# Kernel optimization log

Measured on AMD Instinct MI355X. Metric: run time of the kernel, lower is better.

Reference implementation:

```python
import jax, jax.numpy as jnp
import numpy as np
from jax import lax

B, T, S = 64, 4096, 64


def setup_inputs() -> dict:
    key = jax.random.key(0)
    k1, k2, k3 = jax.random.split(key, 3)
    transition_potentials = jax.random.normal(k1, (S, S), dtype=jnp.float32)
    emission_potentials = jax.random.normal(k2, (B, T, S), dtype=jnp.float32)
    seq_lens = jax.random.randint(k3, (B,), 1, T + 1)
    return {
        "transition_potentials": transition_potentials,
        "emission_potentials": emission_potentials,
        "seq_lens": seq_lens,
    }


def reference(transition_potentials, emission_potentials, seq_lens):
    # potential_normalization='none', potential_scale=1.0 -> normalize is identity.
    # HMM forward algorithm: alpha[t] = logsumexp_i(alpha[t-1,i] + A[i,j]) + emis[t]
    alpha0 = emission_potentials[:, 0, :]  # [B,S]

    def step(alpha_prev, emis_t):
        # alpha_prev: [B,S]; emis_t: [B,S]; transition: [S,S]
        alpha_t = jax.nn.logsumexp(
            alpha_prev[:, :, None] + transition_potentials[None, :, :], axis=1
        ) + emis_t
        return alpha_t, alpha_t

    emis_rest = jnp.moveaxis(emission_potentials[:, 1:, :], 1, 0)  # [T-1,B,S]
    _, alphas = lax.scan(step, alpha0, emis_rest)  # [T-1,B,S]
    alpha = jnp.concatenate([alpha0[None], alphas], axis=0)  # [T,B,S]
    alpha = jnp.moveaxis(alpha, 0, 1)  # [B,T,S]
    log_Z = jax.nn.logsumexp(alpha[:, -1, :], axis=-1)  # [B]
    return alpha, log_Z
```

## Files before the change

kernel.cpp:

```cpp
#include <hip/hip_runtime.h>
#include <hip/hip_bf16.h>


#define BB 64
#define TT 4096
#define SS 64
#define C_CH 128
#define LL 32
#define WARM 24
#define PF 8

typedef __attribute__((ext_vector_type(4))) short bh4;
typedef __attribute__((ext_vector_type(4))) float f32x4;

#define LOG2E 1.44269504088896340736f
#define LN2F  0.69314718055994530942f

__device__ __forceinline__ float fexp2(float x) {
#if __has_builtin(__builtin_amdgcn_exp2f)
    return __builtin_amdgcn_exp2f(x);
#else
    return exp2f(x);
#endif
}
__device__ __forceinline__ float flog2(float x) {
#if __has_builtin(__builtin_amdgcn_logf)
    return __builtin_amdgcn_logf(x);
#else
    return log2f(x);
#endif
}
__device__ __forceinline__ float bpermf(int idx, float v) {
    return __uint_as_float((unsigned)__builtin_amdgcn_ds_bpermute(idx, (int)__float_as_uint(v)));
}
__device__ __forceinline__ int pack_bf16(float x, float y) {
    __hip_bfloat162 h = __float22bfloat162_rn(make_float2(x, y));
    int r; __builtin_memcpy(&r, &h, 4); return r;
}
union PB2 { int i[2]; bh4 v; };

__device__ __forceinline__ f32x4 mfma16(bh4 a, bh4 b, f32x4 c) {
#if __has_builtin(__builtin_amdgcn_mfma_f32_16x16x16bf16_1k)
    return __builtin_amdgcn_mfma_f32_16x16x16bf16_1k(a, b, c, 0, 0, 0);
#else
    asm("v_mfma_f32_16x16x16_bf16 %0, %1, %2, %0" : "+v"(c) : "v"(a), "v"(b));
    return c;
#endif
}

__device__ __forceinline__ float do_step(f32x4 (&al2)[4], const f32x4 (&er)[4],
                                         const bh4 (&Af)[4][4],
                                         float M2, int idxM) {
    bh4 Bf[4];
    #pragma unroll
    for (int kb = 0; kb < 4; ++kb) {
        PB2 pb;
        pb.i[0] = pack_bf16(fexp2(al2[kb].x - M2), fexp2(al2[kb].y - M2));
        pb.i[1] = pack_bf16(fexp2(al2[kb].z - M2), fexp2(al2[kb].w - M2));
        Bf[kb] = pb.v;
    }

    float M2n = 0.f;
    #pragma unroll
    for (int jt = 0; jt < 4; ++jt) {
        f32x4 d0 = {0.f, 0.f, 0.f, 0.f};
        f32x4 d1 = {0.f, 0.f, 0.f, 0.f};
        d0 = mfma16(Af[jt][0], Bf[0], d0);
        d1 = mfma16(Af[jt][1], Bf[1], d1);
        d0 = mfma16(Af[jt][2], Bf[2], d0);
        d1 = mfma16(Af[jt][3], Bf[3], d1);
        f32x4 d = d0 + d1;
        al2[jt].x = fmaf(er[jt].x, LOG2E, M2) + flog2(d.x);
        al2[jt].y = fmaf(er[jt].y, LOG2E, M2) + flog2(d.y);
        al2[jt].z = fmaf(er[jt].z, LOG2E, M2) + flog2(d.z);
        al2[jt].w = fmaf(er[jt].w, LOG2E, M2) + flog2(d.w);
        if (jt == 0) M2n = bpermf(idxM, al2[0].x);
    }
    return M2n;
}

__device__ __forceinline__ void load_row(f32x4 (&dst)[4],
                                         const float* __restrict__ eb,
                                         int t, int off) {
    const float* p = eb + (t & (TT - 1)) * SS + off;
    #pragma unroll
    for (int jt = 0; jt < 4; ++jt)
        dst[jt] = *(const f32x4*)(p + 16 * jt);
}

__global__ __launch_bounds__(64)
__attribute__((amdgpu_waves_per_eu(1, 1)))
void hmm_phaseA(const float* __restrict__ trans,
                const float* __restrict__ emis,
                float* __restrict__ out,
                float* __restrict__ ws_warm,
                float* __restrict__ ws_bound) {
    const int lane = threadIdx.x;
    const int n = lane & 15, q = lane >> 4;
    const int w = blockIdx.x;
    const int b = w >> 3, cg = w & 7;
    const int c = 16 * cg + n;
    const bool is_c0 = (c == 0);
    const int off = 4 * q;

    bh4 Af[4][4];
    #pragma unroll
    for (int jt = 0; jt < 4; ++jt)
        #pragma unroll
        for (int kb = 0; kb < 4; ++kb) {
            float v0 = __expf(trans[(16 * kb + 4 * q + 0) * SS + 16 * jt + n]);
            float v1 = __expf(trans[(16 * kb + 4 * q + 1) * SS + 16 * jt + n]);
            float v2 = __expf(trans[(16 * kb + 4 * q + 2) * SS + 16 * jt + n]);
            float v3 = __expf(trans[(16 * kb + 4 * q + 3) * SS + 16 * jt + n]);
            PB2 pb;
            pb.i[0] = pack_bf16(v0, v1);
            pb.i[1] = pack_bf16(v2, v3);
            Af[jt][kb] = pb.v;
        }

    const int idxM = n << 2;

    const float* eb = emis + (size_t)b * TT * SS;
    float*       ob = out  + (size_t)b * TT * SS;

    const int t0 = LL * c - (WARM + 1);

    f32x4 al2[4], e0[4], ebuf[PF][4];
    load_row(al2, eb, t0, off);
    #pragma unroll
    for (int jt = 0; jt < 4; ++jt) al2[jt] = al2[jt] * LOG2E;
    load_row(e0, eb, 0, off);
    #pragma unroll
    for (int k = 0; k < PF; ++k) load_row(ebuf[k], eb, t0 + 1 + k, off);

    float M2 = bpermf(idxM, al2[0].x);

    #pragma unroll 1
    for (int g = 0; g < 3; ++g) {
        #pragma unroll
        for (int k = 0; k < PF; ++k) {
            int s = PF * g + k + 1;
            f32x4 er[4];
            #pragma unroll
            for (int jt = 0; jt < 4; ++jt) er[jt] = ebuf[k][jt];
            load_row(ebuf[k], eb, t0 + s + PF, off);
            M2 = do_step(al2, er, Af, M2, idxM);
        }
    }
    if (lane < 16)
        ws_warm[b * C_CH + 16 * cg + lane] = al2[0].x * LN2F;

    #pragma unroll 1
    for (int g = 0; g < 4; ++g) {
        #pragma unroll
        for (int k = 0; k < PF; ++k) {
            int s = WARM + 1 + PF * g + k;
            f32x4 er[4];
            #pragma unroll
            for (int jt = 0; jt < 4; ++jt) er[jt] = ebuf[k][jt];
            load_row(ebuf[k], eb, t0 + s + PF, off);
            M2 = do_step(al2, er, Af, M2, idxM);
            if (k == 0 && g == 0) {
                if (is_c0) {
                    #pragma unroll
                    for (int jt = 0; jt < 4; ++jt) al2[jt] = e0[jt] * LOG2E;
                }
                if (cg == 0)
                    M2 = bpermf(idxM, al2[0].x);
            }
            float* p = ob + (t0 + s) * SS + off;
            #pragma unroll
            for (int jt = 0; jt < 4; ++jt)
                *(f32x4*)(p + 16 * jt) = al2[jt] * LN2F;
        }
    }
    if (lane < 16)
        ws_bound[b * C_CH + 16 * cg + lane] = al2[0].x * LN2F;
}

__global__ __launch_bounds__(256)
void hmm_phaseC(float* __restrict__ out,
                const float* __restrict__ ws_warm,
                const float* __restrict__ ws_bound) {
    const int b = blockIdx.x, c = blockIdx.y, tid = threadIdx.x;
    __shared__ float sd[C_CH];

    if (tid < C_CH) {
        float d = 0.f;
        if (tid > 0)
            d = ws_bound[b * C_CH + tid - 1] - ws_warm[b * C_CH + tid];
        sd[tid] = d;
    }
    __syncthreads();
    #pragma unroll
    for (int off = 1; off < C_CH; off <<= 1) {
        float v = 0.f;
        if (tid >= off && tid < C_CH) v = sd[tid - off];
        __syncthreads();
        if (tid >= off && tid < C_CH) sd[tid] += v;
        __syncthreads();
    }
    const float delta = sd[c];

    float4* p4 = (float4*)(out + (size_t)b * TT * SS + (size_t)c * LL * SS);
    float4 last;
    #pragma unroll
    for (int i = 0; i < 2; ++i) {
        int idx = tid + 256 * i;
        float4 v = p4[idx];
        v.x += delta; v.y += delta; v.z += delta; v.w += delta;
        p4[idx] = v;
        last = v;
    }

    if (c == C_CH - 1 && tid >= 240) {
        float mx = fmaxf(fmaxf(last.x, last.y), fmaxf(last.z, last.w));
        #pragma unroll
        for (int off = 8; off >= 1; off >>= 1)
            mx = fmaxf(mx, __shfl_xor(mx, off, 64));
        float sv = __expf(last.x - mx) + __expf(last.y - mx)
                 + __expf(last.z - mx) + __expf(last.w - mx);
        #pragma unroll
        for (int off = 8; off >= 1; off >>= 1)
            sv += __shfl_xor(sv, off, 64);
        if (tid == 240)
            out[(size_t)BB * TT * SS + b] = mx + __logf(sv);
    }
}

extern "C" void kernel_launch(void* const* d_in, const int* in_sizes, int n_in,
                              void* d_out, int out_size, void* d_ws, size_t ws_size,
                              hipStream_t stream) {
    const float* trans = (const float*)d_in[0];
    const float* emis  = (const float*)d_in[1];
    float* out = (float*)d_out;

    float* ws_warm  = (float*)d_ws;
    float* ws_bound = ws_warm + BB * C_CH;

    hmm_phaseA<<<dim3(BB * 8), dim3(64), 0, stream>>>(trans, emis, out,
                                                      ws_warm, ws_bound);
    hmm_phaseC<<<dim3(BB, C_CH), dim3(256), 0, stream>>>(out, ws_warm, ws_bound);
}
```

Measured before the change: 155.1 us.

## Stage emissions via async global-to-LDS loads and coalesce output stores through LDS

The per-lane register prefetch of emission rows is replaced with a triple-buffered LDS ring. It is filled by global_load_lds with an XOR swizzle, so each wave fetches 4-row panels for all 16 chunks in coalesced bursts, paced by explicit vmcnt waits. Output alphas are also written to a swizzled LDS staging area and stored back in coalesced bursts, instead of scattered per-chunk row stores. This targets latency and uncoalesced access on the scattered per-chunk rows. In exchange it uses 64KB of LDS per block and relies on hand-tuned waitcnt counts that must track how loads and stores interleave.

```diff
diff --git a/kernel.cpp b/kernel.cpp
--- a/kernel.cpp
+++ b/kernel.cpp
@@ -8,13 +8,16 @@
 #define C_CH 128
 #define LL 32
 #define WARM 24
-#define PF 8
+#define SLOTF 4096
+#define OUTF  12288
 
 typedef __attribute__((ext_vector_type(4))) short bh4;
 typedef __attribute__((ext_vector_type(4))) float f32x4;
 
 #define LOG2E 1.44269504088896340736f
 #define LN2F  0.69314718055994530942f
+
+#define WAITV(N) asm volatile("s_waitcnt vmcnt(" #N ")" ::: "memory")
 
 __device__ __forceinline__ float fexp2(float x) {
 #if __has_builtin(__builtin_amdgcn_exp2f)
@@ -59,7 +62,6 @@
         pb.i[1] = pack_bf16(fexp2(al2[kb].z - M2), fexp2(al2[kb].w - M2));
         Bf[kb] = pb.v;
     }
-
     float M2n = 0.f;
     #pragma unroll
     for (int jt = 0; jt < 4; ++jt) {
@@ -95,8 +97,11 @@
                 float* __restrict__ out,
                 float* __restrict__ ws_warm,
                 float* __restrict__ ws_bound) {
+    __shared__ float sm[16384];
+
     const int lane = threadIdx.x;
     const int n = lane & 15, q = lane >> 4;
+    const int rl = lane >> 4, ul = lane & 15;
     const int w = blockIdx.x;
     const int b = w >> 3, cg = w & 7;
     const int c = 16 * cg + n;
@@ -125,55 +130,107 @@
 
     const int t0 = LL * c - (WARM + 1);
 
-    f32x4 al2[4], e0[4], ebuf[PF][4];
+    f32x4 al2[4], e0[4];
     load_row(al2, eb, t0, off);
     #pragma unroll
     for (int jt = 0; jt < 4; ++jt) al2[jt] = al2[jt] * LOG2E;
     load_row(e0, eb, 0, off);
     #pragma unroll
-    for (int k = 0; k < PF; ++k) load_row(ebuf[k], eb, t0 + 1 + k, off);
+    for (int jt = 0; jt < 4; ++jt) e0[jt] = e0[jt] * LOG2E;
 
     float M2 = bpermf(idxM, al2[0].x);
 
+    auto issueL = [&](int pp, int slot) {
+        #pragma unroll
+        for (int i = 0; i < 16; ++i) {
+            int ci = 16 * cg + i;
+            int row = (32 * ci - 24 + 4 * pp + rl) & (TT - 1);
+            const float* g = eb + row * SS + ((ul ^ i) << 2);
+            __builtin_amdgcn_global_load_lds(
+                (const __attribute__((address_space(1))) void*)g,
+                (__attribute__((address_space(3))) void*)&sm[slot * SLOTF + i * 256],
+                16, 0, 0);
+        }
+    };
+    auto read_er = [&](f32x4 (&er)[4], int sb, int r) {
+        #pragma unroll
+        for (int jt = 0; jt < 4; ++jt)
+            er[jt] = *(const f32x4*)&sm[sb + n * 256 + r * 64 + ((((jt << 2) + q) ^ n) << 2)];
+    };
+    auto write_out = [&](int r, const f32x4 (&a)[4]) {
+        #pragma unroll
+        for (int jt = 0; jt < 4; ++jt)
+            *(f32x4*)&sm[OUTF + n * 256 + r * 64 + ((((jt << 2) + q) ^ n) << 2)] = a[jt] * LN2F;
+    };
+    auto store_burst = [&](int pp) {
+        #pragma unroll
+        for (int i = 0; i < 16; ++i) {
+            int ci = 16 * cg + i;
+            f32x4 v = *(const f32x4*)&sm[OUTF + i * 256 + rl * 64 + (ul << 2)];
+            int row = 32 * ci - 24 + 4 * pp + rl;
+            *(f32x4*)(ob + (size_t)row * SS + ((ul ^ i) << 2)) = v;
+        }
+    };
+
+    issueL(0, 0);
+    issueL(1, 1);
+
     #pragma unroll 1
-    for (int g = 0; g < 3; ++g) {
-        #pragma unroll
-        for (int k = 0; k < PF; ++k) {
-            int s = PF * g + k + 1;
+    for (int p = 0; p < 6; ++p) {
+        WAITV(16);
+        __builtin_amdgcn_sched_barrier(0);
+        issueL(p + 2, (p + 2) % 3);
+        const int sb = (p % 3) * SLOTF;
+        #pragma unroll
+        for (int r = 0; r < 4; ++r) {
             f32x4 er[4];
-            #pragma unroll
-            for (int jt = 0; jt < 4; ++jt) er[jt] = ebuf[k][jt];
-            load_row(ebuf[k], eb, t0 + s + PF, off);
+            read_er(er, sb, r);
             M2 = do_step(al2, er, Af, M2, idxM);
         }
     }
     if (lane < 16)
         ws_warm[b * C_CH + 16 * cg + lane] = al2[0].x * LN2F;
 
-    #pragma unroll 1
-    for (int g = 0; g < 4; ++g) {
-        #pragma unroll
-        for (int k = 0; k < PF; ++k) {
-            int s = WARM + 1 + PF * g + k;
+    {
+        WAITV(16);
+        __builtin_amdgcn_sched_barrier(0);
+        issueL(8, 2);
+        const int sb = 0;
+        #pragma unroll
+        for (int r = 0; r < 4; ++r) {
             f32x4 er[4];
-            #pragma unroll
-            for (int jt = 0; jt < 4; ++jt) er[jt] = ebuf[k][jt];
-            load_row(ebuf[k], eb, t0 + s + PF, off);
+            read_er(er, sb, r);
             M2 = do_step(al2, er, Af, M2, idxM);
-            if (k == 0 && g == 0) {
+            if (r == 0) {
                 if (is_c0) {
                     #pragma unroll
-                    for (int jt = 0; jt < 4; ++jt) al2[jt] = e0[jt] * LOG2E;
+                    for (int jt = 0; jt < 4; ++jt) al2[jt] = e0[jt];
                 }
                 if (cg == 0)
                     M2 = bpermf(idxM, al2[0].x);
             }
-            float* p = ob + (t0 + s) * SS + off;
-            #pragma unroll
-            for (int jt = 0; jt < 4; ++jt)
-                *(f32x4*)(p + 16 * jt) = al2[jt] * LN2F;
-        }
-    }
+            write_out(r, al2);
+        }
+        store_burst(6);
+    }
+
+    #pragma unroll 1
+    for (int p = 7; p < 14; ++p) {
+        WAITV(32);
+        __builtin_amdgcn_sched_barrier(0);
+        if (p <= 11)
+            issueL(p + 2, (p + 2) % 3);
+        const int sb = (p % 3) * SLOTF;
+        #pragma unroll
+        for (int r = 0; r < 4; ++r) {
+            f32x4 er[4];
+            read_er(er, sb, r);
+            M2 = do_step(al2, er, Af, M2, idxM);
+            write_out(r, al2);
+        }
+        store_burst(p);
+    }
+
     if (lane < 16)
         ws_bound[b * C_CH + 16 * cg + lane] = al2[0].x * LN2F;
 }
```

After: 155.0 us. No clear change (-0.0%).

## Run HMM forward recursion in linear probability space with fixed scaling

Applied to the files above, without the earlier changes.

Replaces the per-step log-space recursion, with its max subtraction, cross-lane bpermute and exp/log on the critical path, by a linear-domain recursion. Transition exponentials are pre-scaled by 1/64 and emissions are exponentiated off the dependency chain. Log is applied only at output time, with a known per-step offset. This shortens the serial dependency chain per timestep, but relies on the fixed scale keeping values inside the fp32/bf16 range for these input statistics, so it risks overflow or underflow on other inputs.

```diff
diff --git a/kernel.cpp b/kernel.cpp
--- a/kernel.cpp
+++ b/kernel.cpp
@@ -30,9 +30,6 @@
     return log2f(x);
 #endif
 }
-__device__ __forceinline__ float bpermf(int idx, float v) {
-    return __uint_as_float((unsigned)__builtin_amdgcn_ds_bpermute(idx, (int)__float_as_uint(v)));
-}
 __device__ __forceinline__ int pack_bf16(float x, float y) {
     __hip_bfloat162 h = __float22bfloat162_rn(make_float2(x, y));
     int r; __builtin_memcpy(&r, &h, 4); return r;
@@ -48,19 +45,16 @@
 #endif
 }
 
-__device__ __forceinline__ float do_step(f32x4 (&al2)[4], const f32x4 (&er)[4],
-                                         const bh4 (&Af)[4][4],
-                                         float M2, int idxM) {
+__device__ __forceinline__ void do_step(f32x4 (&vv)[4], const f32x4 (&eE)[4],
+                                        const bh4 (&Af)[4][4]) {
     bh4 Bf[4];
     #pragma unroll
     for (int kb = 0; kb < 4; ++kb) {
         PB2 pb;
-        pb.i[0] = pack_bf16(fexp2(al2[kb].x - M2), fexp2(al2[kb].y - M2));
-        pb.i[1] = pack_bf16(fexp2(al2[kb].z - M2), fexp2(al2[kb].w - M2));
+        pb.i[0] = pack_bf16(vv[kb].x, vv[kb].y);
+        pb.i[1] = pack_bf16(vv[kb].z, vv[kb].w);
         Bf[kb] = pb.v;
     }
-
-    float M2n = 0.f;
     #pragma unroll
     for (int jt = 0; jt < 4; ++jt) {
         f32x4 d0 = {0.f, 0.f, 0.f, 0.f};
@@ -70,13 +64,8 @@
         d0 = mfma16(Af[jt][2], Bf[2], d0);
         d1 = mfma16(Af[jt][3], Bf[3], d1);
         f32x4 d = d0 + d1;
-        al2[jt].x = fmaf(er[jt].x, LOG2E, M2) + flog2(d.x);
-        al2[jt].y = fmaf(er[jt].y, LOG2E, M2) + flog2(d.y);
-        al2[jt].z = fmaf(er[jt].z, LOG2E, M2) + flog2(d.z);
-        al2[jt].w = fmaf(er[jt].w, LOG2E, M2) + flog2(d.w);
-        if (jt == 0) M2n = bpermf(idxM, al2[0].x);
-    }
-    return M2n;
+        vv[jt] = d * eE[jt];
+    }
 }
 
 __device__ __forceinline__ void load_row(f32x4 (&dst)[4],
@@ -108,74 +97,99 @@
     for (int jt = 0; jt < 4; ++jt)
         #pragma unroll
         for (int kb = 0; kb < 4; ++kb) {
-            float v0 = __expf(trans[(16 * kb + 4 * q + 0) * SS + 16 * jt + n]);
-            float v1 = __expf(trans[(16 * kb + 4 * q + 1) * SS + 16 * jt + n]);
-            float v2 = __expf(trans[(16 * kb + 4 * q + 2) * SS + 16 * jt + n]);
-            float v3 = __expf(trans[(16 * kb + 4 * q + 3) * SS + 16 * jt + n]);
+            float v0 = __expf(trans[(16 * kb + 4 * q + 0) * SS + 16 * jt + n]) * 0.015625f;
+            float v1 = __expf(trans[(16 * kb + 4 * q + 1) * SS + 16 * jt + n]) * 0.015625f;
+            float v2 = __expf(trans[(16 * kb + 4 * q + 2) * SS + 16 * jt + n]) * 0.015625f;
+            float v3 = __expf(trans[(16 * kb + 4 * q + 3) * SS + 16 * jt + n]) * 0.015625f;
             PB2 pb;
             pb.i[0] = pack_bf16(v0, v1);
             pb.i[1] = pack_bf16(v2, v3);
             Af[jt][kb] = pb.v;
         }
 
-    const int idxM = n << 2;
-
     const float* eb = emis + (size_t)b * TT * SS;
     float*       ob = out  + (size_t)b * TT * SS;
 
     const int t0 = LL * c - (WARM + 1);
 
-    f32x4 al2[4], e0[4], ebuf[PF][4];
-    load_row(al2, eb, t0, off);
-    #pragma unroll
-    for (int jt = 0; jt < 4; ++jt) al2[jt] = al2[jt] * LOG2E;
-    load_row(e0, eb, 0, off);
+    const float cL = is_c0 ? (-150.0f * LN2F) : 0.0f;
+
+    f32x4 vv[4], e0v[4], ebuf[PF][4];
+    {
+        f32x4 a0[4], z0[4];
+        load_row(a0, eb, t0, off);
+        load_row(z0, eb, 0, off);
+        #pragma unroll
+        for (int jt = 0; jt < 4; ++jt) {
+            vv[jt].x = fexp2(a0[jt].x * LOG2E);
+            vv[jt].y = fexp2(a0[jt].y * LOG2E);
+            vv[jt].z = fexp2(a0[jt].z * LOG2E);
+            vv[jt].w = fexp2(a0[jt].w * LOG2E);
+            e0v[jt].x = fexp2(z0[jt].x * LOG2E);
+            e0v[jt].y = fexp2(z0[jt].y * LOG2E);
+            e0v[jt].z = fexp2(z0[jt].z * LOG2E);
+            e0v[jt].w = fexp2(z0[jt].w * LOG2E);
+        }
+    }
     #pragma unroll
     for (int k = 0; k < PF; ++k) load_row(ebuf[k], eb, t0 + 1 + k, off);
-
-    float M2 = bpermf(idxM, al2[0].x);
 
     #pragma unroll 1
     for (int g = 0; g < 3; ++g) {
         #pragma unroll
         for (int k = 0; k < PF; ++k) {
             int s = PF * g + k + 1;
-            f32x4 er[4];
+            f32x4 eE[4];
             #pragma unroll
-            for (int jt = 0; jt < 4; ++jt) er[jt] = ebuf[k][jt];
+            for (int jt = 0; jt < 4; ++jt) {
+                eE[jt].x = fexp2(ebuf[k][jt].x * LOG2E);
+                eE[jt].y = fexp2(ebuf[k][jt].y * LOG2E);
+                eE[jt].z = fexp2(ebuf[k][jt].z * LOG2E);
+                eE[jt].w = fexp2(ebuf[k][jt].w * LOG2E);
+            }
             load_row(ebuf[k], eb, t0 + s + PF, off);
-            M2 = do_step(al2, er, Af, M2, idxM);
+            do_step(vv, eE, Af);
         }
     }
     if (lane < 16)
-        ws_warm[b * C_CH + 16 * cg + lane] = al2[0].x * LN2F;
+        ws_warm[b * C_CH + 16 * cg + lane] =
+            fmaf(flog2(vv[0].x), LN2F, 144.0f * LN2F + cL);
 
     #pragma unroll 1
     for (int g = 0; g < 4; ++g) {
         #pragma unroll
         for (int k = 0; k < PF; ++k) {
             int s = WARM + 1 + PF * g + k;
-            f32x4 er[4];
+            f32x4 eE[4];
             #pragma unroll
-            for (int jt = 0; jt < 4; ++jt) er[jt] = ebuf[k][jt];
+            for (int jt = 0; jt < 4; ++jt) {
+                eE[jt].x = fexp2(ebuf[k][jt].x * LOG2E);
+                eE[jt].y = fexp2(ebuf[k][jt].y * LOG2E);
+                eE[jt].z = fexp2(ebuf[k][jt].z * LOG2E);
+                eE[jt].w = fexp2(ebuf[k][jt].w * LOG2E);
+            }
             load_row(ebuf[k], eb, t0 + s + PF, off);
-            M2 = do_step(al2, er, Af, M2, idxM);
-            if (k == 0 && g == 0) {
-                if (is_c0) {
-                    #pragma unroll
-                    for (int jt = 0; jt < 4; ++jt) al2[jt] = e0[jt] * LOG2E;
-                }
-                if (cg == 0)
-                    M2 = bpermf(idxM, al2[0].x);
-            }
+            do_step(vv, eE, Af);
+            if (k == 0 && g == 0 && is_c0) {
+                #pragma unroll
+                for (int jt = 0; jt < 4; ++jt) vv[jt] = e0v[jt];
+            }
+            const float cs = 6.0f * (float)s * LN2F + cL;
             float* p = ob + (t0 + s) * SS + off;
             #pragma unroll
-            for (int jt = 0; jt < 4; ++jt)
-                *(f32x4*)(p + 16 * jt) = al2[jt] * LN2F;
+            for (int jt = 0; jt < 4; ++jt) {
+                f32x4 a;
+                a.x = fmaf(flog2(vv[jt].x), LN2F, cs);
+                a.y = fmaf(flog2(vv[jt].y), LN2F, cs);
+                a.z = fmaf(flog2(vv[jt].z), LN2F, cs);
+                a.w = fmaf(flog2(vv[jt].w), LN2F, cs);
+                *(f32x4*)(p + 16 * jt) = a;
+            }
         }
     }
     if (lane < 16)
-        ws_bound[b * C_CH + 16 * cg + lane] = al2[0].x * LN2F;
+        ws_bound[b * C_CH + 16 * cg + lane] =
+            fmaf(flog2(vv[0].x), LN2F, 336.0f * LN2F + cL);
 }
 
 __global__ __launch_bounds__(256)
```

Measured after the change: 153.5 us. No clear change (-1.0%).
